# Kernel tuning notes

Measured on AMD Instinct MI355X. Metric: run time of the kernel, lower is better.

## Reference

```python
import jax, jax.numpy as jnp
import numpy as np

# Complete binary tree: B trees, L leaves each, processed level-synchronously.
B, L, IN_DIM, MEM = 64, 1024, 300, 256


def setup_inputs() -> dict:
    key = jax.random.key(0)
    ks = jax.random.split(key, 6)
    s = 0.05
    embs = jax.random.normal(ks[0], (B, L, IN_DIM), dtype=jnp.float32)
    # Leaf module: c = cx(x); h = sigmoid(ox(x)) * tanh(c)
    Wcx = jax.random.normal(ks[1], (MEM, IN_DIM), dtype=jnp.float32) * s
    bcx = jnp.zeros((MEM,), jnp.float32)
    Wox = jax.random.normal(ks[2], (MEM, IN_DIM), dtype=jnp.float32) * s
    box = jnp.zeros((MEM,), jnp.float32)
    # Composer: 4 gates (i, lf, rf, u), each gate = Linear(lh) + Linear(rh).
    # Stacked: Wl/Wr have shape [4, MEM, MEM]; biases [4, MEM].
    Wl = jax.random.normal(ks[3], (4, MEM, MEM), dtype=jnp.float32) * s
    bl = jnp.zeros((4, MEM), jnp.float32)
    Wr = jax.random.normal(ks[4], (4, MEM, MEM), dtype=jnp.float32) * s
    br = jnp.zeros((4, MEM), jnp.float32)
    return dict(embs=embs, Wcx=Wcx, bcx=bcx, Wox=Wox, box=box,
                Wl=Wl, bl=bl, Wr=Wr, br=br)


def reference(embs, Wcx, bcx, Wox, box, Wl, bl, Wr, br):
    # Leaf module (BinaryTreeLeafModule.forward), vectorized over all leaves.
    c = jnp.einsum('blx,mx->blm', embs, Wcx) + bcx          # [B, L, MEM]
    o = jax.nn.sigmoid(jnp.einsum('blx,mx->blm', embs, Wox) + box)
    h = o * jnp.tanh(c)

    bias = bl + br                                          # [4, MEM]
    n = c.shape[1]
    while n > 1:  # log2(L) levels, static unrolled loop
        lc, rc = c[:, 0::2], c[:, 1::2]                     # [B, n/2, MEM]
        lh, rh = h[:, 0::2], h[:, 1::2]
        # All 4 gate pre-activations fused: [B, n/2, 4, MEM]
        g = (jnp.einsum('bnm,gom->bngo', lh, Wl)
             + jnp.einsum('bnm,gom->bngo', rh, Wr) + bias)
        i = jax.nn.sigmoid(g[..., 0, :])
        lf = jax.nn.sigmoid(g[..., 1, :])
        rf = jax.nn.sigmoid(g[..., 2, :])
        u = jnp.tanh(g[..., 3, :])
        c = i * u + lf * lc + rf * rc                       # composer cell
        h = jnp.tanh(c)                                     # gate_output=False path
        n //= 2

    # Root state (tree.state = (c, h)); stacked as [2, B, MEM]
    return jnp.stack([c[:, 0], h[:, 0]])
```

## Files before the change

### kernel.cpp

```cpp
#include <hip/hip_runtime.h>
#include <hip/hip_bf16.h>


typedef __attribute__((ext_vector_type(8))) short bf16x8;
typedef __attribute__((ext_vector_type(4))) float f32x4;

__device__ __forceinline__ float fsig(float x)  { return 1.f / (1.f + __expf(-x)); }
__device__ __forceinline__ float ftanh(float x) { return 1.f - 2.f / (__expf(2.f * x) + 1.f); }
__device__ __forceinline__ ushort f2bf(float x) {
    __hip_bfloat16 b = __float2bfloat16(x);
    return *reinterpret_cast<ushort*>(&b);
}

__device__ __forceinline__ void gld_lds16(const void* g, void* l) {
    __builtin_amdgcn_global_load_lds((const __attribute__((address_space(1))) void*)g,
                                     (__attribute__((address_space(3))) void*)l, 16, 0, 0);
}

__global__ void conv_embs(const float* __restrict__ E, ushort* __restrict__ Eb)
{
    int tid = blockIdx.x * 256 + threadIdx.x;
    int row = tid / 80;
    int k = (tid - row * 80) * 4;
    float4 v = make_float4(0.f, 0.f, 0.f, 0.f);
    if (k < 300) v = *(const float4*)(E + (size_t)row * 300 + k);
    ushort4 o;
    o.x = f2bf(v.x); o.y = f2bf(v.y); o.z = f2bf(v.z); o.w = f2bf(v.w);
    *(ushort4*)(Eb + (size_t)row * 320 + k) = o;
}

__global__ void pack_leaf_k(const float* __restrict__ Wcx, const float* __restrict__ Wox,
                            const float* __restrict__ bcx, const float* __restrict__ box,
                            ushort* __restrict__ Wb, float* __restrict__ bp)
{
    int idx = blockIdx.x * 256 + threadIdx.x;
    if (idx < 163840) {
        int e = idx & 7, slot = (idx >> 3) & 3, o = (idx >> 5) & 255;
        int g = (idx >> 13) & 1, t = idx >> 14;
        int q = slot ^ ((o >> 1) & 3);
        int k = t * 32 + q * 8 + e;
        float v = 0.f;
        if (k < 300) v = g ? Wox[o * 300 + k] : Wcx[o * 300 + k];
        Wb[idx] = f2bf(v);
    }
    if (idx < 512) {
        int g = idx >> 8, o = idx & 255;
        bp[idx] = g ? box[o] : bcx[o];
    }
}

__global__ void pack_level_k(const float* __restrict__ Wl, const float* __restrict__ Wr,
                             const float* __restrict__ bl, const float* __restrict__ br,
                             ushort* __restrict__ Wb, float* __restrict__ bp)
{
    int idx = blockIdx.x * 256 + threadIdx.x;
    if (idx < 524288) {
        int e = idx & 7, slot = (idx >> 3) & 3, o = (idx >> 5) & 255;
        int g = (idx >> 13) & 3, t = idx >> 15;
        int q = slot ^ ((o >> 1) & 3);
        int k = t * 32 + q * 8 + e;
        float v = (k < 256) ? Wl[(g * 256 + o) * 256 + k]
                            : Wr[(g * 256 + o) * 256 + (k - 256)];
        Wb[idx] = f2bf(v);
    }
    if (idx < 1024) bp[idx] = bl[idx] + br[idx];
}


template<int NG, int HALVES, int MODE>
__global__ __launch_bounds__(256, 4)
void mfma_gemm(const ushort* __restrict__ A,
               const ushort* __restrict__ Wb,
               const float* __restrict__ bp,
               const float* __restrict__ Cprev,
               float* __restrict__ c_out,
               ushort* __restrict__ h_out,
               float* __restrict__ hf_out,
               int M)
{
    constexpr int K = HALVES * 32;
    constexpr int OW = 128 / NG;
    __shared__ __align__(16) ushort As[2][512 * 8];
    __shared__ __align__(16) ushort Bs[2][512 * 8];

    const int tid = threadIdx.x;
    const int wid = tid >> 6, ln = tid & 63;
    const int lq = ln >> 4, lr = ln & 15;
    const int wm = wid >> 1, wn = wid & 1;
    const int rowBlk = blockIdx.x * 128;
    const int o0 = blockIdx.y * OW;

    f32x4 acc[4][4];
#pragma unroll
    for (int m = 0; m < 4; ++m)
#pragma unroll
        for (int f = 0; f < 4; ++f) acc[m][f] = f32x4{0.f, 0.f, 0.f, 0.f};

    const int ar0 = tid >> 2,  as0 = tid & 3;
    const int ar1 = ar0 + 64;
    const int aq0 = (as0 - ((ar0 >> 1) & 3)) & 3;
    const int aq1 = (as0 - ((ar1 >> 1) & 3)) & 3;
    const ushort* aP0 = A + (size_t)min(rowBlk + ar0, M - 1) * K + aq0 * 8;
    const ushort* aP1 = A + (size_t)min(rowBlk + ar1, M - 1) * K + aq1 * 8;
    const int bj0 = tid >> 2,        bs0 = tid & 3;
    const int bj1 = (tid + 256) >> 2;
    const int bg0 = bj0 / OW, bo0 = o0 + (bj0 & (OW - 1));
    const int bg1 = bj1 / OW, bo1 = o0 + (bj1 & (OW - 1));
    const ushort* bP0 = Wb + ((size_t)bg0 * 1024 + bo0 * 4 + bs0) * 8;
    const ushort* bP1 = Wb + ((size_t)bg1 * 1024 + bo1 * 4 + bs0) * 8;
    constexpr size_t BSTR = (size_t)NG * 1024 * 8;

    const int aSw = (lq + ((lr >> 1) & 3)) & 3;
    const int bSw = lq ^ ((lr >> 1) & 3);
    int aOff[4];
#pragma unroll
    for (int m = 0; m < 4; ++m)
        aOff[m] = ((wm * 64 + m * 16 + lr) * 4 + aSw) * 8;
    int bOff[4];
#pragma unroll
    for (int f = 0; f < 4; ++f)
        bOff[f] = ((f * 32 + wn * 16 + lr) * 4 + bSw) * 8;

    gld_lds16(aP0, &As[0][tid * 8]);
    gld_lds16(aP1, &As[0][(tid + 256) * 8]);
    gld_lds16(bP0, &Bs[0][tid * 8]);
    gld_lds16(bP1, &Bs[0][(tid + 256) * 8]);

#pragma unroll
    for (int h = 0; h < HALVES; ++h) {
        __syncthreads();
        const int cur = h & 1;
        if (h + 1 < HALVES) {
            gld_lds16(aP0 + (size_t)(h + 1) * 32, &As[cur ^ 1][tid * 8]);
            gld_lds16(aP1 + (size_t)(h + 1) * 32, &As[cur ^ 1][(tid + 256) * 8]);
            gld_lds16(bP0 + (size_t)(h + 1) * BSTR, &Bs[cur ^ 1][tid * 8]);
            gld_lds16(bP1 + (size_t)(h + 1) * BSTR, &Bs[cur ^ 1][(tid + 256) * 8]);
        }
        bf16x8 a[4];
#pragma unroll
        for (int m = 0; m < 4; ++m)
            a[m] = *(const bf16x8*)&As[cur][aOff[m]];
#pragma unroll
        for (int f = 0; f < 4; ++f) {
            bf16x8 b = *(const bf16x8*)&Bs[cur][bOff[f]];
#pragma unroll
            for (int m = 0; m < 4; ++m)
                acc[m][f] = __builtin_amdgcn_mfma_f32_16x16x32_bf16(a[m], b, acc[m][f], 0, 0, 0);
        }
    }

#pragma unroll
    for (int m = 0; m < 4; ++m) {
        const int row0 = rowBlk + wm * 64 + m * 16 + lq * 4;
        if constexpr (MODE == 0) {
#pragma unroll
            for (int ob = 0; ob < 2; ++ob) {
                const int col = o0 + ob * 32 + wn * 16 + lr;
                const float bc = bp[col], bo = bp[256 + col];
#pragma unroll
                for (int j = 0; j < 4; ++j) {
                    int row = row0 + j;
                    if (row < M) {
                        float cv = acc[m][ob][j] + bc;
                        float ov = acc[m][2 + ob][j] + bo;
                        c_out[(size_t)row * 256 + col] = cv;
                        h_out[(size_t)row * 256 + col] = f2bf(fsig(ov) * ftanh(cv));
                    }
                }
            }
        } else {
            const int col = o0 + wn * 16 + lr;
            const float bi  = bp[col],       blf = bp[256 + col];
            const float brf = bp[512 + col], bu  = bp[768 + col];
#pragma unroll
            for (int j = 0; j < 4; ++j) {
                int row = row0 + j;
                if (row < M) {
                    float gi = fsig(acc[m][0][j] + bi);
                    float lf = fsig(acc[m][1][j] + blf);
                    float rf = fsig(acc[m][2][j] + brf);
                    float gu = ftanh(acc[m][3][j] + bu);
                    float lc = Cprev[(size_t)row * 512 + col];
                    float rc = Cprev[(size_t)row * 512 + 256 + col];
                    float cv = gi * gu + lf * lc + rf * rc;
                    float hv = ftanh(cv);
                    c_out[(size_t)row * 256 + col] = cv;
                    if constexpr (MODE == 2) hf_out[(size_t)row * 256 + col] = hv;
                    else                     h_out[(size_t)row * 256 + col] = f2bf(hv);
                }
            }
        }
    }
}


extern "C" void kernel_launch(void* const* d_in, const int* in_sizes, int n_in,
                              void* d_out, int out_size, void* d_ws, size_t ws_size,
                              hipStream_t stream)
{
    const float* embs = (const float*)d_in[0];
    const float* Wcx  = (const float*)d_in[1];
    const float* bcx  = (const float*)d_in[2];
    const float* Wox  = (const float*)d_in[3];
    const float* box  = (const float*)d_in[4];
    const float* Wl   = (const float*)d_in[5];
    const float* bl   = (const float*)d_in[6];
    const float* Wr   = (const float*)d_in[7];
    const float* br   = (const float*)d_in[8];

    char* p = (char*)d_ws;
    ushort* Wb2 = (ushort*)p;  p += (size_t)524288 * 2;
    ushort* WbL = (ushort*)p;  p += (size_t)163840 * 2;
    float*  bp2 = (float*)p;   p += 1024 * 4;
    float*  bpL = (float*)p;   p += 512 * 4;
    float*  c0  = (float*)p;   p += (size_t)65536 * 256 * 4;
    ushort* h0  = (ushort*)p;  p += (size_t)65536 * 256 * 2;
    char* X = p;
    ushort* embsB = (ushort*)X;
    float*  cA = (float*)X;
    ushort* hA = (ushort*)(X + (size_t)32768 * 256 * 4);
    float*  cB = (float*)(X + (size_t)48 * 1024 * 1024);
    ushort* hB = (ushort*)(X + (size_t)64 * 1024 * 1024);

    conv_embs<<<20480, 256, 0, stream>>>(embs, embsB);
    pack_leaf_k<<<640, 256, 0, stream>>>(Wcx, Wox, bcx, box, WbL, bpL);
    pack_level_k<<<2048, 256, 0, stream>>>(Wl, Wr, bl, br, Wb2, bp2);

    mfma_gemm<2, 10, 0><<<dim3(512, 4), 256, 0, stream>>>(
        embsB, WbL, bpL, nullptr, c0, h0, nullptr, 65536);

    const ushort* hin = h0;
    const float*  cin = c0;
    float*  cping[2] = {cA, cB};
    ushort* hping[2] = {hA, hB};
    int flip = 0;
    for (int np = 512; np >= 1; np >>= 1) {
        int M = 64 * np;
        int gx = (M + 127) / 128;
        if (np == 1) {
            mfma_gemm<4, 16, 2><<<dim3(gx, 8), 256, 0, stream>>>(
                hin, Wb2, bp2, cin, (float*)d_out, nullptr, (float*)d_out + 64 * 256, M);
        } else {
            float* co = cping[flip]; ushort* ho = hping[flip];
            mfma_gemm<4, 16, 1><<<dim3(gx, 8), 256, 0, stream>>>(
                hin, Wb2, bp2, cin, co, ho, nullptr, M);
            cin = co; hin = ho; flip ^= 1;
        }
    }
}
```

Before: 299.4 us.

## Fuse prep kernels and run last seven tree levels in one per-tree kernel

Merges the three weight/embedding packing kernels into one prep launch. After three batched GEMM levels, one block per tree runs the remaining seven levels inside a single tail kernel. That kernel keeps h in swizzled LDS and streams weights directly from global memory. This removes many small, under-occupied launches for the upper levels, but the tail runs only 64 blocks and the c scratch aliases the h0 buffer.

```diff
diff --git a/kernel.cpp b/kernel.cpp
--- a/kernel.cpp
+++ b/kernel.cpp
@@ -17,53 +17,48 @@
                                      (__attribute__((address_space(3))) void*)l, 16, 0, 0);
 }
 
-__global__ void conv_embs(const float* __restrict__ E, ushort* __restrict__ Eb)
-{
-    int tid = blockIdx.x * 256 + threadIdx.x;
-    int row = tid / 80;
-    int k = (tid - row * 80) * 4;
-    float4 v = make_float4(0.f, 0.f, 0.f, 0.f);
-    if (k < 300) v = *(const float4*)(E + (size_t)row * 300 + k);
-    ushort4 o;
-    o.x = f2bf(v.x); o.y = f2bf(v.y); o.z = f2bf(v.z); o.w = f2bf(v.w);
-    *(ushort4*)(Eb + (size_t)row * 320 + k) = o;
-}
-
-__global__ void pack_leaf_k(const float* __restrict__ Wcx, const float* __restrict__ Wox,
-                            const float* __restrict__ bcx, const float* __restrict__ box,
-                            ushort* __restrict__ Wb, float* __restrict__ bp)
-{
-    int idx = blockIdx.x * 256 + threadIdx.x;
-    if (idx < 163840) {
-        int e = idx & 7, slot = (idx >> 3) & 3, o = (idx >> 5) & 255;
-        int g = (idx >> 13) & 1, t = idx >> 14;
+__global__ void prep(const float* __restrict__ Wl,  const float* __restrict__ Wr,
+                     const float* __restrict__ bl,  const float* __restrict__ br,
+                     const float* __restrict__ Wcx, const float* __restrict__ Wox,
+                     const float* __restrict__ bcx, const float* __restrict__ box,
+                     const float* __restrict__ embs,
+                     ushort* __restrict__ Wb2, ushort* __restrict__ WbL,
+                     float* __restrict__ bp2, float* __restrict__ bpL,
+                     ushort* __restrict__ embsB)
+{
+    const int gid = blockIdx.x * 256 + threadIdx.x;
+    for (int i = gid; i < 524288; i += 262144) {
+        int e = i & 7, slot = (i >> 3) & 3, o = (i >> 5) & 255;
+        int g = (i >> 13) & 3, t = i >> 15;
+        int q = slot ^ ((o >> 1) & 3);
+        int k = t * 32 + q * 8 + e;
+        float v = (k < 256) ? Wl[(g * 256 + o) * 256 + k]
+                            : Wr[(g * 256 + o) * 256 + (k - 256)];
+        Wb2[i] = f2bf(v);
+    }
+    if (gid < 163840) {
+        int e = gid & 7, slot = (gid >> 3) & 3, o = (gid >> 5) & 255;
+        int g = (gid >> 13) & 1, t = gid >> 14;
         int q = slot ^ ((o >> 1) & 3);
         int k = t * 32 + q * 8 + e;
         float v = 0.f;
         if (k < 300) v = g ? Wox[o * 300 + k] : Wcx[o * 300 + k];
-        Wb[idx] = f2bf(v);
-    }
-    if (idx < 512) {
-        int g = idx >> 8, o = idx & 255;
-        bp[idx] = g ? box[o] : bcx[o];
-    }
-}
-
-__global__ void pack_level_k(const float* __restrict__ Wl, const float* __restrict__ Wr,
-                             const float* __restrict__ bl, const float* __restrict__ br,
-                             ushort* __restrict__ Wb, float* __restrict__ bp)
-{
-    int idx = blockIdx.x * 256 + threadIdx.x;
-    if (idx < 524288) {
-        int e = idx & 7, slot = (idx >> 3) & 3, o = (idx >> 5) & 255;
-        int g = (idx >> 13) & 3, t = idx >> 15;
-        int q = slot ^ ((o >> 1) & 3);
-        int k = t * 32 + q * 8 + e;
-        float v = (k < 256) ? Wl[(g * 256 + o) * 256 + k]
-                            : Wr[(g * 256 + o) * 256 + (k - 256)];
-        Wb[idx] = f2bf(v);
-    }
-    if (idx < 1024) bp[idx] = bl[idx] + br[idx];
+        WbL[gid] = f2bf(v);
+    }
+    if (gid < 1024) bp2[gid] = bl[gid] + br[gid];
+    if (gid < 512) {
+        int g = gid >> 8, o = gid & 255;
+        bpL[gid] = g ? box[o] : bcx[o];
+    }
+    for (int i = gid; i < 65536 * 80; i += 262144) {
+        int row = i / 80;
+        int k = (i - row * 80) * 4;
+        float4 v = make_float4(0.f, 0.f, 0.f, 0.f);
+        if (k < 300) v = *(const float4*)(embs + (size_t)row * 300 + k);
+        ushort4 o4;
+        o4.x = f2bf(v.x); o4.y = f2bf(v.y); o4.z = f2bf(v.z); o4.w = f2bf(v.w);
+        *(ushort4*)(embsB + (size_t)row * 320 + k) = o4;
+    }
 }
 
 
@@ -75,7 +70,6 @@
                const float* __restrict__ Cprev,
                float* __restrict__ c_out,
                ushort* __restrict__ h_out,
-               float* __restrict__ hf_out,
                int M)
 {
     constexpr int K = HALVES * 32;
@@ -183,14 +177,142 @@
                     float lc = Cprev[(size_t)row * 512 + col];
                     float rc = Cprev[(size_t)row * 512 + 256 + col];
                     float cv = gi * gu + lf * lc + rf * rc;
-                    float hv = ftanh(cv);
                     c_out[(size_t)row * 256 + col] = cv;
-                    if constexpr (MODE == 2) hf_out[(size_t)row * 256 + col] = hv;
-                    else                     h_out[(size_t)row * 256 + col] = f2bf(hv);
+                    h_out[(size_t)row * 256 + col] = f2bf(ftanh(cv));
                 }
             }
         }
     }
+}
+
+
+template<int MC, bool LAST>
+__device__ __forceinline__ void tail_level(
+    const ushort* inb, ushort* outb,
+    const ushort* __restrict__ Wb, const float* __restrict__ bp,
+    const float* __restrict__ cprev, float* __restrict__ cout_,
+    float* __restrict__ dout, int b, int npo)
+{
+    const int tid = threadIdx.x;
+    const int wid = tid >> 6, ln = tid & 63;
+    const int lq = ln >> 4, lr = ln & 15;
+
+#pragma unroll
+    for (int oh = 0; oh < 2; ++oh) {
+        const int ob = wid * 64 + oh * 32;
+        f32x4 acc[MC][2][4];
+#pragma unroll
+        for (int m = 0; m < MC; ++m)
+#pragma unroll
+            for (int of = 0; of < 2; ++of)
+#pragma unroll
+                for (int g = 0; g < 4; ++g) acc[m][of][g] = f32x4{0.f, 0.f, 0.f, 0.f};
+
+        int o_[2], sl_[2];
+#pragma unroll
+        for (int of = 0; of < 2; ++of) {
+            o_[of] = ob + of * 16 + lr;
+            sl_[of] = lq ^ ((o_[of] >> 1) & 3);
+        }
+
+#pragma unroll
+        for (int ks = 0; ks < 16; ++ks) {
+            bf16x8 bfr[2][4];
+#pragma unroll
+            for (int of = 0; of < 2; ++of)
+#pragma unroll
+                for (int g = 0; g < 4; ++g)
+                    bfr[of][g] = *(const bf16x8*)(Wb +
+                        ((size_t)(ks * 4 + g) * 1024 + o_[of] * 4 + sl_[of]) * 8);
+            bf16x8 a[MC];
+#pragma unroll
+            for (int m = 0; m < MC; ++m) {
+                int r = m * 16 + lr;
+                int pr = 2 * r + (ks >> 3);
+                int pc = lq + (ks & 7) * 4;
+                a[m] = *(const bf16x8*)&inb[pr * 256 + ((pc ^ ((pr >> 1) & 7)) * 8)];
+            }
+#pragma unroll
+            for (int of = 0; of < 2; ++of)
+#pragma unroll
+                for (int g = 0; g < 4; ++g)
+#pragma unroll
+                    for (int m = 0; m < MC; ++m)
+                        acc[m][of][g] = __builtin_amdgcn_mfma_f32_16x16x32_bf16(
+                            a[m], bfr[of][g], acc[m][of][g], 0, 0, 0);
+        }
+
+#pragma unroll
+        for (int m = 0; m < MC; ++m) {
+#pragma unroll
+            for (int of = 0; of < 2; ++of) {
+                const int col = ob + of * 16 + lr;
+                const float bi  = bp[col],       blf = bp[256 + col];
+                const float brf = bp[512 + col], bu  = bp[768 + col];
+#pragma unroll
+                for (int j = 0; j < 4; ++j) {
+                    int row = m * 16 + lq * 4 + j;
+                    if (row < npo) {
+                        float gi = fsig(acc[m][of][0][j] + bi);
+                        float lf = fsig(acc[m][of][1][j] + blf);
+                        float rf = fsig(acc[m][of][2][j] + brf);
+                        float gu = ftanh(acc[m][of][3][j] + bu);
+                        float lc = cprev[(size_t)(2 * row) * 256 + col];
+                        float rc = cprev[(size_t)(2 * row + 1) * 256 + col];
+                        float cv = gi * gu + lf * lc + rf * rc;
+                        float hv = ftanh(cv);
+                        if (LAST) {
+                            dout[b * 256 + col] = cv;
+                            dout[16384 + b * 256 + col] = hv;
+                        } else {
+                            cout_[row * 256 + col] = cv;
+                            outb[row * 256 + (((col >> 3) ^ ((row >> 1) & 7)) * 8) + (col & 7)] = f2bf(hv);
+                        }
+                    }
+                }
+            }
+        }
+    }
+}
+
+__global__ __launch_bounds__(256, 1)
+void tail_lstm(const ushort* __restrict__ hin,
+               const float* __restrict__ cin,
+               const ushort* __restrict__ Wb,
+               const float* __restrict__ bp,
+               float* __restrict__ cscr,
+               float* __restrict__ dout)
+{
+    __shared__ __align__(16) ushort P0[128 * 256];
+    __shared__ __align__(16) ushort P1[64 * 256];
+
+    const int b = blockIdx.x;
+    const int tid = threadIdx.x;
+
+    for (int ct = tid; ct < 4096; ct += 256) {
+        int pr = ct >> 5, pc = ct & 31;
+        bf16x8 v = *(const bf16x8*)(hin + ((size_t)(b * 128 + pr) * 256 + pc * 8));
+        *(bf16x8*)&P0[pr * 256 + ((pc ^ ((pr >> 1) & 7)) * 8)] = v;
+    }
+    __syncthreads();
+
+    float* c0p = cscr + (size_t)b * 64 * 256;
+    float* c1p = cscr + (size_t)(64 + b) * 64 * 256;
+    const float* cin_b = cin + (size_t)b * 128 * 256;
+
+    tail_level<4, false>(P0, P1, Wb, bp, cin_b, c0p, nullptr, b, 64);
+    __syncthreads();
+    tail_level<2, false>(P1, P0, Wb, bp, c0p, c1p, nullptr, b, 32);
+    __syncthreads();
+    tail_level<1, false>(P0, P1, Wb, bp, c1p, c0p, nullptr, b, 16);
+    __syncthreads();
+    tail_level<1, false>(P1, P0, Wb, bp, c0p, c1p, nullptr, b, 8);
+    __syncthreads();
+    tail_level<1, false>(P0, P1, Wb, bp, c1p, c0p, nullptr, b, 4);
+    __syncthreads();
+    tail_level<1, false>(P1, P0, Wb, bp, c0p, c1p, nullptr, b, 2);
+    __syncthreads();
+    tail_level<1, true>(P0, P1, Wb, bp, c1p, nullptr, dout, b, 1);
 }
 
 
@@ -214,6 +336,7 @@
     float*  bp2 = (float*)p;   p += 1024 * 4;
     float*  bpL = (float*)p;   p += 512 * 4;
     float*  c0  = (float*)p;   p += (size_t)65536 * 256 * 4;
+    float*  cscr= (float*)p;
     ushort* h0  = (ushort*)p;  p += (size_t)65536 * 256 * 2;
     char* X = p;
     ushort* embsB = (ushort*)X;
@@ -222,29 +345,19 @@
     float*  cB = (float*)(X + (size_t)48 * 1024 * 1024);
     ushort* hB = (ushort*)(X + (size_t)64 * 1024 * 1024);
 
-    conv_embs<<<20480, 256, 0, stream>>>(embs, embsB);
-    pack_leaf_k<<<640, 256, 0, stream>>>(Wcx, Wox, bcx, box, WbL, bpL);
-    pack_level_k<<<2048, 256, 0, stream>>>(Wl, Wr, bl, br, Wb2, bp2);
+    prep<<<1024, 256, 0, stream>>>(Wl, Wr, bl, br, Wcx, Wox, bcx, box, embs,
+                                   Wb2, WbL, bp2, bpL, embsB);
 
     mfma_gemm<2, 10, 0><<<dim3(512, 4), 256, 0, stream>>>(
-        embsB, WbL, bpL, nullptr, c0, h0, nullptr, 65536);
-
-    const ushort* hin = h0;
-    const float*  cin = c0;
-    float*  cping[2] = {cA, cB};
-    ushort* hping[2] = {hA, hB};
-    int flip = 0;
-    for (int np = 512; np >= 1; np >>= 1) {
-        int M = 64 * np;
-        int gx = (M + 127) / 128;
-        if (np == 1) {
-            mfma_gemm<4, 16, 2><<<dim3(gx, 8), 256, 0, stream>>>(
-                hin, Wb2, bp2, cin, (float*)d_out, nullptr, (float*)d_out + 64 * 256, M);
-        } else {
-            float* co = cping[flip]; ushort* ho = hping[flip];
-            mfma_gemm<4, 16, 1><<<dim3(gx, 8), 256, 0, stream>>>(
-                hin, Wb2, bp2, cin, co, ho, nullptr, M);
-            cin = co; hin = ho; flip ^= 1;
-        }
-    }
-}
+        embsB, WbL, bpL, nullptr, c0, h0, 65536);
+
+    mfma_gemm<4, 16, 1><<<dim3(256, 8), 256, 0, stream>>>(
+        h0, Wb2, bp2, c0, cA, hA, 32768);
+    mfma_gemm<4, 16, 1><<<dim3(128, 8), 256, 0, stream>>>(
+        hA, Wb2, bp2, cA, cB, hB, 16384);
+    mfma_gemm<4, 16, 1><<<dim3(64, 8), 256, 0, stream>>>(
+        hB, Wb2, bp2, cB, cA, hA, 8192);
+
+    tail_lstm<<<64, 256, 0, stream>>>(
+        hA, cA, Wb2, bp2, cscr, (float*)d_out);
+}
```

Measured after the change: 650.7 us. +117.3%, slower.
